# Kernel tuning notes

Measured on AMD Instinct MI355X. Metric: run time of the kernel, lower is better.

## Reference

```python
import jax, jax.numpy as jnp
import numpy as np

BN_EPS = 1e-5


def _bn(h, gamma, beta, mean, var):
    return (h - mean) * jax.lax.rsqrt(var + BN_EPS) * gamma + beta


def _gin_conv(x, edge_index, edge_weight, Wa, ba, g, be, m, v, Wb, bb):
    # GINConv: (1+eps)*x + sum_j w_ij * x_j, eps=0; then MLP: Linear->BN->ReLU->Linear
    src, dst = edge_index[0], edge_index[1]
    msg = x[src] * edge_weight[:, None]                      # [E, C]
    agg = jax.ops.segment_sum(msg, dst, num_segments=x.shape[0])  # [N, C]
    h = x + agg
    h = h @ Wa + ba
    h = jax.nn.relu(_bn(h, g, be, m, v))
    return h @ Wb + bb


def setup_inputs() -> dict:
    key = jax.random.key(0)
    ks = jax.random.split(key, 16)
    N, E, C_IN, C_OUT, H = 100000, 1600000, 128, 64, 32
    x = jax.random.normal(ks[0], (N, C_IN), dtype=jnp.float32)
    edge_index = jax.random.randint(ks[1], (2, E), 0, N, dtype=jnp.int32)
    edge_weight = jax.random.uniform(ks[2], (E,), dtype=jnp.float32)
    s1 = 1.0 / np.sqrt(C_IN)
    s2 = 1.0 / np.sqrt(H)
    return {
        "x": x,
        "edge_weight": edge_weight,
        "W1a": jax.random.normal(ks[3], (C_IN, H), dtype=jnp.float32) * s1,
        "b1a": jnp.zeros((H,), jnp.float32),
        "g1": jnp.ones((H,), jnp.float32),
        "be1": jnp.zeros((H,), jnp.float32),
        "m1": jax.random.normal(ks[4], (H,), dtype=jnp.float32) * 0.1,
        "v1": jax.random.uniform(ks[5], (H,), dtype=jnp.float32) + 0.5,
        "W1b": jax.random.normal(ks[6], (H, H), dtype=jnp.float32) * s2,
        "b1b": jnp.zeros((H,), jnp.float32),
        "W2a": jax.random.normal(ks[7], (H, C_OUT), dtype=jnp.float32) * s2,
        "b2a": jnp.zeros((C_OUT,), jnp.float32),
        "g2": jnp.ones((C_OUT,), jnp.float32),
        "be2": jnp.zeros((C_OUT,), jnp.float32),
        "m2": jax.random.normal(ks[8], (C_OUT,), dtype=jnp.float32) * 0.1,
        "v2": jax.random.uniform(ks[9], (C_OUT,), dtype=jnp.float32) + 0.5,
        "W2b": jax.random.normal(ks[10], (C_OUT, C_OUT), dtype=jnp.float32) * (1.0 / np.sqrt(C_OUT)),
        "b2b": jnp.zeros((C_OUT,), jnp.float32),
        "edge_index": edge_index,
    }


def reference(x, edge_weight, W1a, b1a, g1, be1, m1, v1, W1b, b1b,
              W2a, b2a, g2, be2, m2, v2, W2b, b2b, edge_index):
    # eval mode: dropout(p=0.6) is identity, BN uses running stats
    h = jax.nn.relu(_gin_conv(x, edge_index, edge_weight,
                              W1a, b1a, g1, be1, m1, v1, W1b, b1b))
    out = _gin_conv(h, edge_index, edge_weight,
                    W2a, b2a, g2, be2, m2, v2, W2b, b2b)
    return out
```

## Files before the change

### kernel.cpp

```cpp
#include <hip/hip_runtime.h>


#define BN_EPS 1e-5f
#define BKT 128
#define BKT_SH 7
#define EPB 4096
#define MAXB 800
#define LDS_E 2560

__device__ __forceinline__ unsigned short f2bf(float f) {
    unsigned u = __float_as_uint(f);
    return (unsigned short)((u + 0x7FFFu + ((u >> 16) & 1u)) >> 16);
}
__device__ __forceinline__ float bflo(unsigned u) { return __uint_as_float(u << 16); }
__device__ __forceinline__ float bfhi(unsigned u) { return __uint_as_float(u & 0xFFFF0000u); }

__device__ __forceinline__ void gacc8(uint4 v, float w, float* acc) {
    acc[0] += bflo(v.x) * w; acc[1] += bfhi(v.x) * w;
    acc[2] += bflo(v.y) * w; acc[3] += bfhi(v.y) * w;
    acc[4] += bflo(v.z) * w; acc[5] += bfhi(v.z) * w;
    acc[6] += bflo(v.w) * w; acc[7] += bfhi(v.w) * w;
}

__device__ __forceinline__ void gather_seg8(const unsigned short* __restrict__ tab,
                                            const int2* __restrict__ epack,
                                            int e, int end, int c0, float* acc) {
    long long q0 = 0, q1 = 0, q2 = 0, q3 = 0;
    if (e + 4 <= end) {
        q0 = __builtin_nontemporal_load((const long long*)&epack[e + 0]);
        q1 = __builtin_nontemporal_load((const long long*)&epack[e + 1]);
        q2 = __builtin_nontemporal_load((const long long*)&epack[e + 2]);
        q3 = __builtin_nontemporal_load((const long long*)&epack[e + 3]);
    }
    for (; e + 8 <= end; e += 4) {
        int s0 = (int)q0, s1 = (int)q1, s2 = (int)q2, s3 = (int)q3;
        float w0 = __int_as_float((int)(q0 >> 32));
        float w1 = __int_as_float((int)(q1 >> 32));
        float w2 = __int_as_float((int)(q2 >> 32));
        float w3 = __int_as_float((int)(q3 >> 32));
        uint4 v0 = *(const uint4*)&tab[(size_t)s0 * 32 + c0];
        uint4 v1 = *(const uint4*)&tab[(size_t)s1 * 32 + c0];
        uint4 v2 = *(const uint4*)&tab[(size_t)s2 * 32 + c0];
        uint4 v3 = *(const uint4*)&tab[(size_t)s3 * 32 + c0];
        q0 = __builtin_nontemporal_load((const long long*)&epack[e + 4]);
        q1 = __builtin_nontemporal_load((const long long*)&epack[e + 5]);
        q2 = __builtin_nontemporal_load((const long long*)&epack[e + 6]);
        q3 = __builtin_nontemporal_load((const long long*)&epack[e + 7]);
        gacc8(v0, w0, acc); gacc8(v1, w1, acc);
        gacc8(v2, w2, acc); gacc8(v3, w3, acc);
    }
    if (e + 4 <= end) {
        int s0 = (int)q0, s1 = (int)q1, s2 = (int)q2, s3 = (int)q3;
        float w0 = __int_as_float((int)(q0 >> 32));
        float w1 = __int_as_float((int)(q1 >> 32));
        float w2 = __int_as_float((int)(q2 >> 32));
        float w3 = __int_as_float((int)(q3 >> 32));
        uint4 v0 = *(const uint4*)&tab[(size_t)s0 * 32 + c0];
        uint4 v1 = *(const uint4*)&tab[(size_t)s1 * 32 + c0];
        uint4 v2 = *(const uint4*)&tab[(size_t)s2 * 32 + c0];
        uint4 v3 = *(const uint4*)&tab[(size_t)s3 * 32 + c0];
        gacc8(v0, w0, acc); gacc8(v1, w1, acc);
        gacc8(v2, w2, acc); gacc8(v3, w3, acc);
        e += 4;
    }
    for (; e < end; ++e) {
        long long q = __builtin_nontemporal_load((const long long*)&epack[e]);
        int sn = (int)q;
        float w = __int_as_float((int)(q >> 32));
        uint4 v = *(const uint4*)&tab[(size_t)sn * 32 + c0];
        gacc8(v, w, acc);
    }
}

__global__ __launch_bounds__(256) void gemm1_kernel(const float* __restrict__ x,
                                                    const float* __restrict__ W,
                                                    unsigned short* __restrict__ y1b,
                                                    int* __restrict__ gcur,
                                                    int N, int ncur) {
    __shared__ float xs[32][129];
    __shared__ float ws[128 * 32];
    int t = threadIdx.x;
    if (t == 0) {
        int b0 = blockIdx.x * 8;
        #pragma unroll
        for (int j = 0; j < 8; ++j)
            if (b0 + j < ncur) gcur[b0 + j] = 0;
    }
    for (int i = t; i < 4096; i += 256) ws[i] = W[i];
    int row0 = blockIdx.x * 32;
    for (int j = 0; j < 4; ++j) {
        int f4 = t + j * 256;
        int r  = f4 >> 5;
        int kc = (f4 & 31) << 2;
        if (row0 + r < N) {
            float4 v = *(const float4*)&x[(size_t)(row0 + r) * 128 + kc];
            xs[r][kc + 0] = v.x; xs[r][kc + 1] = v.y;
            xs[r][kc + 2] = v.z; xs[r][kc + 3] = v.w;
        }
    }
    __syncthreads();
    int r  = t >> 3;
    int c0 = (t & 7) << 2;
    if (row0 + r >= N) return;
    float a0 = 0.f, a1 = 0.f, a2 = 0.f, a3 = 0.f;
    #pragma unroll 8
    for (int k = 0; k < 128; ++k) {
        float xv = xs[r][k];
        const float* wr = &ws[k * 32 + c0];
        a0 += xv * wr[0]; a1 += xv * wr[1]; a2 += xv * wr[2]; a3 += xv * wr[3];
    }
    ushort4 o = {f2bf(a0), f2bf(a1), f2bf(a2), f2bf(a3)};
    *(ushort4*)&y1b[(size_t)(row0 + r) * 32 + c0] = o;
}

__global__ __launch_bounds__(256) void stage_kernel(const int* __restrict__ ei,
                                                    const float* __restrict__ ew,
                                                    int* __restrict__ gcur,
                                                    int2* __restrict__ staged,
                                                    int E, int cap, int NBUCK) {
    __shared__ int hist[MAXB], base_[MAXB], curs[MAXB], gbase[MAXB];
    __shared__ int2 data[EPB];
    __shared__ unsigned short bslot[EPB];
    int t  = threadIdx.x;
    int e0 = blockIdx.x * EPB;
    int cnt = min(EPB, E - e0);
    for (int i = t; i < MAXB; i += 256) hist[i] = 0;
    __syncthreads();
    for (int i = t; i < cnt; i += 256) {
        int d = ei[(size_t)E + e0 + i];
        atomicAdd(&hist[d >> BKT_SH], 1);
    }
    __syncthreads();
    int lo = t * 4;
    int vb[4];
    int s = 0;
    #pragma unroll
    for (int j = 0; j < 4; ++j) {
        int idx = lo + j;
        vb[j] = (idx < MAXB) ? hist[idx] : 0;
        s += vb[j];
    }
    gbase[t] = s;
    __syncthreads();
    for (int off = 1; off < 256; off <<= 1) {
        int x = (t >= off) ? gbase[t - off] : 0;
        __syncthreads();
        gbase[t] += x;
        __syncthreads();
    }
    int excl = gbase[t] - s;
    #pragma unroll
    for (int j = 0; j < 4; ++j) {
        int idx = lo + j;
        if (idx < MAXB) { base_[idx] = excl; curs[idx] = excl; }
        excl += vb[j];
    }
    __syncthreads();
    for (int i = t; i < cnt; i += 256) {
        int sn = ei[e0 + i];
        int d  = ei[(size_t)E + e0 + i];
        float w = ew[e0 + i];
        int b = d >> BKT_SH, dl = d & (BKT - 1);
        int pos = atomicAdd(&curs[b], 1);
        data[pos]  = make_int2((dl << 20) | sn, __float_as_int(w));
        bslot[pos] = (unsigned short)b;
    }
    __syncthreads();
    for (int b = t; b < NBUCK; b += 256) {
        int c = hist[b];
        gbase[b] = c ? atomicAdd(&gcur[b * 16], c) : 0;
    }
    __syncthreads();
    for (int i = t; i < cnt; i += 256) {
        int b  = bslot[i];
        int gp = gbase[b] + (i - base_[b]);
        if (gp < cap) staged[(size_t)b * cap + gp] = data[i];
    }
}

__global__ __launch_bounds__(256) void refill_kernel(const int2* __restrict__ staged,
                                                     const int* __restrict__ gcur,
                                                     int2* __restrict__ epack,
                                                     int2* __restrict__ row_se,
                                                     int N, int cap) {
    __shared__ int2 ebuf[LDS_E];
    __shared__ int hist[BKT];
    __shared__ int curs[BKT];
    int b = blockIdx.x, t = threadIdx.x;
    int cnt  = min(gcur[b * 16], cap);
    int base = b * cap;
    size_t e0 = (size_t)b * cap;
    if (t < BKT) hist[t] = 0;
    __syncthreads();
    for (int i = t; i < cnt; i += 256) {
        int2 p = staged[e0 + i];
        ebuf[i] = p;
        atomicAdd(&hist[p.x >> 20], 1);
    }
    __syncthreads();
    if (t < BKT) curs[t] = hist[t];
    __syncthreads();
    for (int off = 1; off < BKT; off <<= 1) {
        int y = (t < BKT && t >= off) ? curs[t - off] : 0;
        __syncthreads();
        if (t < BKT) curs[t] += y;
        __syncthreads();
    }
    if (t < BKT) {
        int excl = curs[t] - hist[t];
        int node = (b << BKT_SH) + t;
        if (node < N) row_se[node] = make_int2(base + excl, base + excl + hist[t]);
        curs[t] = excl;
    }
    __syncthreads();
    for (int i = t; i < cnt; i += 256) {
        int2 p = ebuf[i];
        int dl = p.x >> 20;
        int pos = base + atomicAdd(&curs[dl], 1);
        epack[pos] = make_int2(p.x & 0xFFFFF, p.y);
    }
}

__global__ __launch_bounds__(256) void layer1_kernel(
    const unsigned short* __restrict__ y1b, const int2* __restrict__ row_se,
    const int2* __restrict__ epack,
    const float* __restrict__ b1a, const float* __restrict__ g1,
    const float* __restrict__ be1, const float* __restrict__ m1,
    const float* __restrict__ v1, const float* __restrict__ W1b,
    const float* __restrict__ b1b, unsigned short* __restrict__ h1b, int N) {
    __shared__ float w1b[1024];
    __shared__ float t1s[64][33];
    int t = threadIdx.x;
    for (int i = t; i < 1024; i += 256) w1b[i] = W1b[i];
    int g = t >> 2, l = t & 3;
    int node = blockIdx.x * 64 + g;
    int c0 = l << 3;
    bool act = node < N;
    float acc[8] = {0.f, 0.f, 0.f, 0.f, 0.f, 0.f, 0.f, 0.f};
    if (act) {
        int2 se = row_se[node];
        gather_seg8(y1b, epack, se.x, se.y, c0, acc);
        uint4 sv = *(const uint4*)&y1b[(size_t)node * 32 + c0];
        gacc8(sv, 1.f, acc);
        #pragma unroll
        for (int j = 0; j < 8; ++j) {
            int c = c0 + j;
            float scale = g1[c] * rsqrtf(v1[c] + BN_EPS);
            t1s[g][c] = fmaxf((acc[j] + b1a[c] - m1[c]) * scale + be1[c], 0.f);
        }
    }
    __syncthreads();
    if (act) {
        float a[8];
        #pragma unroll
        for (int j = 0; j < 8; ++j) a[j] = b1b[c0 + j];
        #pragma unroll
        for (int k = 0; k < 32; ++k) {
            float tv = t1s[g][k];
            const float* wr = &w1b[k * 32 + c0];
            #pragma unroll
            for (int j = 0; j < 8; ++j) a[j] += tv * wr[j];
        }
        unsigned long long p0 = 0, p1 = 0;
        #pragma unroll
        for (int j = 0; j < 4; ++j)
            p0 |= (unsigned long long)f2bf(fmaxf(a[j], 0.f)) << (16 * j);
        #pragma unroll
        for (int j = 0; j < 4; ++j)
            p1 |= (unsigned long long)f2bf(fmaxf(a[4 + j], 0.f)) << (16 * j);
        __builtin_nontemporal_store(p0, (unsigned long long*)&h1b[(size_t)node * 32 + c0 + 0]);
        __builtin_nontemporal_store(p1, (unsigned long long*)&h1b[(size_t)node * 32 + c0 + 4]);
    }
}

__global__ __launch_bounds__(256) void layer2a_kernel(
    const unsigned short* __restrict__ h1b, const int2* __restrict__ row_se,
    const int2* __restrict__ epack,
    const float* __restrict__ W2a, const float* __restrict__ b2a,
    const float* __restrict__ g2, const float* __restrict__ be2,
    const float* __restrict__ m2, const float* __restrict__ v2,
    unsigned short* __restrict__ t2b, int N) {
    __shared__ float w2a[2048];
    __shared__ float s1s[64][33];
    __shared__ float sc2s[64], sh2s[64];
    int t = threadIdx.x;
    for (int i = t; i < 2048; i += 256) w2a[i] = W2a[i];
    if (t < 64) {
        float sc = g2[t] * rsqrtf(v2[t] + BN_EPS);
        sc2s[t] = sc;
        sh2s[t] = (b2a[t] - m2[t]) * sc + be2[t];
    }
    int g = t >> 2, l = t & 3;
    int node = blockIdx.x * 64 + g;
    int c0 = l << 3;
    bool act = node < N;
    float acc[8] = {0.f, 0.f, 0.f, 0.f, 0.f, 0.f, 0.f, 0.f};
    if (act) {
        int2 se = row_se[node];
        gather_seg8(h1b, epack, se.x, se.y, c0, acc);
        uint4 sv = *(const uint4*)&h1b[(size_t)node * 32 + c0];
        gacc8(sv, 1.f, acc);
        #pragma unroll
        for (int j = 0; j < 8; ++j) s1s[g][c0 + j] = acc[j];
    }
    __syncthreads();
    if (act) {
        int d0 = l << 4;
        float a[16];
        #pragma unroll
        for (int j = 0; j < 16; ++j) a[j] = 0.f;
        #pragma unroll
        for (int k = 0; k < 32; ++k) {
            float sv = s1s[g][k];
            const float* wr = &w2a[k * 64 + d0];
            #pragma unroll
            for (int j = 0; j < 16; ++j) a[j] += sv * wr[j];
        }
        unsigned long long pk[4] = {0, 0, 0, 0};
        #pragma unroll
        for (int j = 0; j < 16; ++j) {
            int c = d0 + j;
            float o = fmaxf(a[j] * sc2s[c] + sh2s[c], 0.f);
            pk[j >> 2] |= (unsigned long long)f2bf(o) << (16 * (j & 3));
        }
        #pragma unroll
        for (int q = 0; q < 4; ++q)
            __builtin_nontemporal_store(pk[q],
                (unsigned long long*)&t2b[(size_t)node * 64 + d0 + 4 * q]);
    }
}

__global__ __launch_bounds__(256) void final_kernel(const unsigned short* __restrict__ t2b,
                                                    const float* __restrict__ W2b,
                                                    const float* __restrict__ b2b,
                                                    float* __restrict__ out, int N) {
    __shared__ float w2b[4096];
    __shared__ float t2s[32][68];
    int t = threadIdx.x;
    for (int i = t; i < 4096; i += 256) w2b[i] = W2b[i];
    int g = t >> 3, l = t & 7;
    int node = blockIdx.x * 32 + g;
    int c0 = l << 3;
    bool act = node < N;
    if (act) {
        uint4 v = *(const uint4*)&t2b[(size_t)node * 64 + c0];
        t2s[g][c0 + 0] = bflo(v.x); t2s[g][c0 + 1] = bfhi(v.x);
        t2s[g][c0 + 2] = bflo(v.y); t2s[g][c0 + 3] = bfhi(v.y);
        t2s[g][c0 + 4] = bflo(v.z); t2s[g][c0 + 5] = bfhi(v.z);
        t2s[g][c0 + 6] = bflo(v.w); t2s[g][c0 + 7] = bfhi(v.w);
    }
    __syncthreads();
    if (act) {
        float a[8];
        #pragma unroll
        for (int j = 0; j < 8; ++j) a[j] = b2b[c0 + j];
        #pragma unroll 8
        for (int k = 0; k < 64; ++k) {
            float tv = t2s[g][k];
            const float* wr = &w2b[k * 64 + c0];
            float4 w0 = *(const float4*)wr;
            float4 w1 = *(const float4*)(wr + 4);
            a[0] += tv * w0.x; a[1] += tv * w0.y; a[2] += tv * w0.z; a[3] += tv * w0.w;
            a[4] += tv * w1.x; a[5] += tv * w1.y; a[6] += tv * w1.z; a[7] += tv * w1.w;
        }
        *(float4*)&out[(size_t)node * 64 + c0 + 0] = *(float4*)&a[0];
        *(float4*)&out[(size_t)node * 64 + c0 + 4] = *(float4*)&a[4];
    }
}

extern "C" void kernel_launch(void* const* d_in, const int* in_sizes, int n_in,
                              void* d_out, int out_size, void* d_ws, size_t ws_size,
                              hipStream_t stream) {
    const float* x   = (const float*)d_in[0];
    const float* ew  = (const float*)d_in[1];
    const float* W1a = (const float*)d_in[2];
    const float* b1a = (const float*)d_in[3];
    const float* g1  = (const float*)d_in[4];
    const float* be1 = (const float*)d_in[5];
    const float* m1  = (const float*)d_in[6];
    const float* v1  = (const float*)d_in[7];
    const float* W1b = (const float*)d_in[8];
    const float* b1b = (const float*)d_in[9];
    const float* W2a = (const float*)d_in[10];
    const float* b2a = (const float*)d_in[11];
    const float* g2  = (const float*)d_in[12];
    const float* be2 = (const float*)d_in[13];
    const float* m2  = (const float*)d_in[14];
    const float* v2  = (const float*)d_in[15];
    const float* W2b = (const float*)d_in[16];
    const float* b2b = (const float*)d_in[17];
    const int*   ei  = (const int*)d_in[18];

    const int N = in_sizes[0] / 128;
    const int E = in_sizes[1];
    const int NBUCK = (N + BKT - 1) >> BKT_SH;
    const int NCUR  = NBUCK * 16;

    unsigned short* y1b = (unsigned short*)d_ws;
    int2*  row_se  = (int2*)(y1b + (size_t)N * 32);
    int*   gcur    = (int*)(row_se + N);
    int2*  epack   = (int2*)(gcur + NCUR + 16);
    size_t fixed_bytes = (char*)epack - (char*)d_ws;
    size_t avail = (ws_size > fixed_bytes) ? (ws_size - fixed_bytes) : 0;
    int cap = (int)((avail / (2 * sizeof(int2))) / NBUCK);
    cap &= ~63;
    if (cap > LDS_E) cap = LDS_E;
    int2* staged = epack + (size_t)NBUCK * cap;
    unsigned short* h1b = (unsigned short*)staged;
    unsigned short* t2b = h1b + (size_t)N * 32;

    gemm1_kernel<<<(N + 31) / 32, 256, 0, stream>>>(x, W1a, y1b, gcur, N, NCUR);
    stage_kernel<<<(E + EPB - 1) / EPB, 256, 0, stream>>>(ei, ew, gcur, staged, E, cap, NBUCK);
    refill_kernel<<<NBUCK, 256, 0, stream>>>(staged, gcur, epack, row_se, N, cap);
    layer1_kernel<<<(N + 63) / 64, 256, 0, stream>>>(y1b, row_se, epack,
                                                     b1a, g1, be1, m1, v1, W1b, b1b, h1b, N);
    layer2a_kernel<<<(N + 63) / 64, 256, 0, stream>>>(h1b, row_se, epack,
                                                      W2a, b2a, g2, be2, m2, v2, t2b, N);
    final_kernel<<<(N + 31) / 32, 256, 0, stream>>>(t2b, W2b, b2b, (float*)d_out, N);
}
```

Measured before the change: 172.6 us.

## Retile gemm1, widen stage blocks, drop post-gather block barriers

```diff
diff --git a/kernel.cpp b/kernel.cpp
--- a/kernel.cpp
+++ b/kernel.cpp
@@ -77,18 +77,18 @@
                                                     unsigned short* __restrict__ y1b,
                                                     int* __restrict__ gcur,
                                                     int N, int ncur) {
-    __shared__ float xs[32][129];
+    __shared__ float xs[64][129];
     __shared__ float ws[128 * 32];
     int t = threadIdx.x;
     if (t == 0) {
-        int b0 = blockIdx.x * 8;
-        #pragma unroll
-        for (int j = 0; j < 8; ++j)
+        int b0 = blockIdx.x * 16;
+        #pragma unroll
+        for (int j = 0; j < 16; ++j)
             if (b0 + j < ncur) gcur[b0 + j] = 0;
     }
     for (int i = t; i < 4096; i += 256) ws[i] = W[i];
-    int row0 = blockIdx.x * 32;
-    for (int j = 0; j < 4; ++j) {
+    int row0 = blockIdx.x * 64;
+    for (int j = 0; j < 8; ++j) {
         int f4 = t + j * 256;
         int r  = f4 >> 5;
         int kc = (f4 & 31) << 2;
@@ -99,64 +99,60 @@
         }
     }
     __syncthreads();
-    int r  = t >> 3;
-    int c0 = (t & 7) << 2;
+    int r  = t >> 2;
+    int c0 = (t & 3) << 3;
     if (row0 + r >= N) return;
-    float a0 = 0.f, a1 = 0.f, a2 = 0.f, a3 = 0.f;
+    float a[8] = {0.f, 0.f, 0.f, 0.f, 0.f, 0.f, 0.f, 0.f};
     #pragma unroll 8
     for (int k = 0; k < 128; ++k) {
         float xv = xs[r][k];
         const float* wr = &ws[k * 32 + c0];
-        a0 += xv * wr[0]; a1 += xv * wr[1]; a2 += xv * wr[2]; a3 += xv * wr[3];
-    }
-    ushort4 o = {f2bf(a0), f2bf(a1), f2bf(a2), f2bf(a3)};
-    *(ushort4*)&y1b[(size_t)(row0 + r) * 32 + c0] = o;
-}
-
-__global__ __launch_bounds__(256) void stage_kernel(const int* __restrict__ ei,
+        #pragma unroll
+        for (int j = 0; j < 8; ++j) a[j] += xv * wr[j];
+    }
+    ushort4 o0 = {f2bf(a[0]), f2bf(a[1]), f2bf(a[2]), f2bf(a[3])};
+    ushort4 o1 = {f2bf(a[4]), f2bf(a[5]), f2bf(a[6]), f2bf(a[7])};
+    *(ushort4*)&y1b[(size_t)(row0 + r) * 32 + c0 + 0] = o0;
+    *(ushort4*)&y1b[(size_t)(row0 + r) * 32 + c0 + 4] = o1;
+}
+
+__global__ __launch_bounds__(512) void stage_kernel(const int* __restrict__ ei,
                                                     const float* __restrict__ ew,
                                                     int* __restrict__ gcur,
                                                     int2* __restrict__ staged,
                                                     int E, int cap, int NBUCK) {
-    __shared__ int hist[MAXB], base_[MAXB], curs[MAXB], gbase[MAXB];
+    __shared__ int hist[MAXB], base_[MAXB], curs[MAXB];
+    __shared__ int gbase[MAXB];
     __shared__ int2 data[EPB];
     __shared__ unsigned short bslot[EPB];
     int t  = threadIdx.x;
     int e0 = blockIdx.x * EPB;
     int cnt = min(EPB, E - e0);
-    for (int i = t; i < MAXB; i += 256) hist[i] = 0;
-    __syncthreads();
-    for (int i = t; i < cnt; i += 256) {
+    for (int i = t; i < MAXB; i += 512) hist[i] = 0;
+    __syncthreads();
+    for (int i = t; i < cnt; i += 512) {
         int d = ei[(size_t)E + e0 + i];
         atomicAdd(&hist[d >> BKT_SH], 1);
     }
     __syncthreads();
-    int lo = t * 4;
-    int vb[4];
-    int s = 0;
-    #pragma unroll
-    for (int j = 0; j < 4; ++j) {
-        int idx = lo + j;
-        vb[j] = (idx < MAXB) ? hist[idx] : 0;
-        s += vb[j];
-    }
+    int lo = t * 2;
+    int v0 = (lo + 0 < MAXB) ? hist[lo + 0] : 0;
+    int v1 = (lo + 1 < MAXB) ? hist[lo + 1] : 0;
+    int s = v0 + v1;
     gbase[t] = s;
     __syncthreads();
-    for (int off = 1; off < 256; off <<= 1) {
-        int x = (t >= off) ? gbase[t - off] : 0;
+    for (int off = 1; off < 512; off <<= 1) {
+        int y = (t >= off) ? gbase[t - off] : 0;
         __syncthreads();
-        gbase[t] += x;
+        gbase[t] += y;
         __syncthreads();
     }
     int excl = gbase[t] - s;
-    #pragma unroll
-    for (int j = 0; j < 4; ++j) {
-        int idx = lo + j;
-        if (idx < MAXB) { base_[idx] = excl; curs[idx] = excl; }
-        excl += vb[j];
-    }
-    __syncthreads();
-    for (int i = t; i < cnt; i += 256) {
+    if (lo + 0 < MAXB) { base_[lo + 0] = excl; curs[lo + 0] = excl; }
+    excl += v0;
+    if (lo + 1 < MAXB) { base_[lo + 1] = excl; curs[lo + 1] = excl; }
+    __syncthreads();
+    for (int i = t; i < cnt; i += 512) {
         int sn = ei[e0 + i];
         int d  = ei[(size_t)E + e0 + i];
         float w = ew[e0 + i];
@@ -166,12 +162,12 @@
         bslot[pos] = (unsigned short)b;
     }
     __syncthreads();
-    for (int b = t; b < NBUCK; b += 256) {
+    for (int b = t; b < NBUCK; b += 512) {
         int c = hist[b];
         gbase[b] = c ? atomicAdd(&gcur[b * 16], c) : 0;
     }
     __syncthreads();
-    for (int i = t; i < cnt; i += 256) {
+    for (int i = t; i < cnt; i += 512) {
         int b  = bslot[i];
         int gp = gbase[b] + (i - base_[b]);
         if (gp < cap) staged[(size_t)b * cap + gp] = data[i];
@@ -232,6 +228,7 @@
     __shared__ float t1s[64][33];
     int t = threadIdx.x;
     for (int i = t; i < 1024; i += 256) w1b[i] = W1b[i];
+    __syncthreads();
     int g = t >> 2, l = t & 3;
     int node = blockIdx.x * 64 + g;
     int c0 = l << 3;
@@ -249,7 +246,7 @@
             t1s[g][c] = fmaxf((acc[j] + b1a[c] - m1[c]) * scale + be1[c], 0.f);
         }
     }
-    __syncthreads();
+    asm volatile("" ::: "memory");
     if (act) {
         float a[8];
         #pragma unroll
@@ -290,6 +287,7 @@
         sc2s[t] = sc;
         sh2s[t] = (b2a[t] - m2[t]) * sc + be2[t];
     }
+    __syncthreads();
     int g = t >> 2, l = t & 3;
     int node = blockIdx.x * 64 + g;
     int c0 = l << 3;
@@ -303,7 +301,7 @@
         #pragma unroll
         for (int j = 0; j < 8; ++j) s1s[g][c0 + j] = acc[j];
     }
-    __syncthreads();
+    asm volatile("" ::: "memory");
     if (act) {
         int d0 = l << 4;
         float a[16];
@@ -409,8 +407,8 @@
     unsigned short* h1b = (unsigned short*)staged;
     unsigned short* t2b = h1b + (size_t)N * 32;
 
-    gemm1_kernel<<<(N + 31) / 32, 256, 0, stream>>>(x, W1a, y1b, gcur, N, NCUR);
-    stage_kernel<<<(E + EPB - 1) / EPB, 256, 0, stream>>>(ei, ew, gcur, staged, E, cap, NBUCK);
+    gemm1_kernel<<<(N + 63) / 64, 256, 0, stream>>>(x, W1a, y1b, gcur, N, NCUR);
+    stage_kernel<<<(E + EPB - 1) / EPB, 512, 0, stream>>>(ei, ew, gcur, staged, E, cap, NBUCK);
     refill_kernel<<<NBUCK, 256, 0, stream>>>(staged, gcur, epack, row_se, N, cap);
     layer1_kernel<<<(N + 63) / 64, 256, 0, stream>>>(y1b, row_se, epack,
                                                      b1a, g1, be1, m1, v1, W1b, b1b, h1b, N);
```

After: 166.8 us. 1.03x faster.
